# Kernel optimization log

Hardware: AMD Instinct MI355X
Metric: run time of the kernel (lower is better)

The kernel has to match this reference:

```python
import jax, jax.numpy as jnp
import numpy as np

B, H, T, TE = 48, 256, 512, 256  # batch*nodes, hidden=node_dim, timesteps, time_emb_dim


def timestep_embedding(ts, dim, max_positions=10000):
    half = dim // 2
    freqs = jnp.exp(jnp.arange(half, dtype=jnp.float32) * (-np.log(max_positions) / (half - 1)))
    e = ts.astype(jnp.float32)[:, None] * freqs[None, :]
    return jnp.concatenate([jnp.sin(e), jnp.cos(e)], axis=-1)  # [len, dim]


def mlp2(x, W1, b1, W2, b2):
    # 2-layer MLP: Linear -> SiLU -> Linear
    return jax.nn.silu(x @ W1 + b1) @ W2 + b2


def setup_inputs() -> dict:
    key = jax.random.key(0)
    ks = jax.random.split(key, 16)
    s = lambda k, shp, fan: (jax.random.normal(k, shp, dtype=jnp.float32) / np.sqrt(fan))
    return {
        "x": jax.random.normal(ks[0], (B, 3, T), dtype=jnp.float32),
        "h": jax.random.normal(ks[1], (B, H, T), dtype=jnp.float32),
        "qW1": s(ks[2], (H, H), H), "qb1": jnp.zeros((H,), jnp.float32),
        "qW2": s(ks[3], (H, H), H), "qb2": jnp.zeros((H,), jnp.float32),
        "kW1": s(ks[4], (H, H), H), "kb1": jnp.zeros((H,), jnp.float32),
        "kW2": s(ks[5], (H, H), H), "kb2": jnp.zeros((H,), jnp.float32),
        "vW1": s(ks[6], (H, H), H), "vb1": jnp.zeros((H,), jnp.float32),
        "vW2": s(ks[7], (H, H), H), "vb2": jnp.zeros((H,), jnp.float32),
        "xW1": s(ks[8], (H, H), H), "xb1": jnp.zeros((H,), jnp.float32),
        "xW2": s(ks[9], (H, 1), H), "xb2": jnp.zeros((1,), jnp.float32),
        "teW": s(ks[10], (TE, H), TE), "teb": jnp.zeros((H,), jnp.float32),
    }


def reference(x, h, qW1, qb1, qW2, qb2, kW1, kb1, kW2, kb2,
              vW1, vb1, vW2, vb2, xW1, xb1, xW2, xb2, teW, teb):
    Bb, _, Tt = x.shape
    rel_range = jnp.arange(-Tt + 1, Tt)
    emb_rel = timestep_embedding(rel_range, teW.shape[0]) @ teW + teb  # [2T-1, H]
    idx = jnp.arange(Tt)[:, None] - jnp.arange(Tt)[None, :] + (Tt - 1)  # [T, T]
    rel_pos = emb_rel[idx]  # [T, T, H]

    hm = h.transpose(0, 2, 1).reshape(Bb * Tt, -1)  # merge_time_dim: [BT, H]
    q = mlp2(hm, qW1, qb1, qW2, qb2)
    k = mlp2(hm, kW1, kb1, kW2, kb2)
    v = mlp2(hm, vW1, vb1, vW2, vb2)
    v_x = mlp2(v, xW1, xb1, xW2, xb2)  # [BT, 1]

    qt = q.reshape(Bb, Tt, -1)   # [B, T, H]
    kt = k.reshape(Bb, Tt, -1)
    vt = v.reshape(Bb, Tt, -1)

    base = jnp.einsum('bth,bsh->bts', qt, kt)  # [B, T, T]
    rel_logits = qt @ emb_rel.T  # [B, T, 2T-1]
    bias_logits = jnp.take_along_axis(
        rel_logits, jnp.broadcast_to(idx[None], (Bb, Tt, Tt)), axis=2)
    alpha = jax.nn.softmax(base + bias_logits, axis=-1)  # [B, T, T]

    std_vs = jnp.einsum('bts,bsh->bht', alpha, vt)       # [B, H, T]
    bias_h = jnp.einsum('bts,tsh->bht', alpha, rel_pos)  # [B, H, T]
    h_new = h + std_vs + bias_h

    # equivariant coord update: sum_s alpha[b,t,s]*(x[b,c,t]-x[b,c,s])*v_x[b,s]
    vx = v_x.reshape(Bb, Tt)               # [B, T]
    w = alpha * vx[:, None, :]             # [B, T, T]
    x_update = x * jnp.sum(w, axis=-1)[:, None, :] - jnp.einsum('bts,bcs->bct', w, x)
    x_new = x + x_update
    return (x_new, h_new)
```

## Files before the change

### kernel.cpp

```cpp
#include <hip/hip_runtime.h>
#include <math.h>

#define NB 48
#define HD 256
#define TS 512

typedef _Float16 f16x8 __attribute__((ext_vector_type(8)));
typedef float    f32x4 __attribute__((ext_vector_type(4)));

__device__ inline unsigned short f2h(float f) {
  union { _Float16 h; unsigned short u; } v; v.h = (_Float16)f; return v.u;
}
__device__ inline float h2f(unsigned short u) {
  union { unsigned short u; _Float16 h; } v; v.u = u; return (float)v.h;
}

#define ETS 1056

__device__ __forceinline__ void gll16(const void* g, void* l) {
  __builtin_amdgcn_global_load_lds(
      (const __attribute__((address_space(1))) unsigned int*)g,
      (__attribute__((address_space(3))) unsigned int*)l, 16, 0, 0);
}

__global__ __launch_bounds__(256) void k_embrel(
    const float* __restrict__ teW, const float* __restrict__ teb,
    unsigned short* __restrict__ embB, unsigned short* __restrict__ embT)
{
  __shared__ float e[256];
  const int r = blockIdx.x;
  const int tid = threadIdx.x;
  if (r == 1023) {
    embB[1023 * 256 + tid] = 0;
    for (int c = 1023; c < ETS; ++c) embT[(size_t)tid * ETS + c] = 0;
    return;
  }
  const float rel = (float)(r - (TS - 1));
  if (tid < 128) {
    float f = expf((float)tid * (-9.210340371976184f / 127.0f));
    float ang = rel * f;
    e[tid] = sinf(ang);
    e[tid + 128] = cosf(ang);
  }
  __syncthreads();
  float acc = teb[tid];
  for (int kk = 0; kk < 256; ++kk)
    acc = fmaf(e[kk], teW[kk * 256 + tid], acc);
  unsigned short hv = f2h(acc);
  embB[r * 256 + tid] = hv;
  embT[(size_t)tid * ETS + r] = hv;
}

__global__ __launch_bounds__(256) void k_prep_h(
    const float* __restrict__ h, unsigned short* __restrict__ hmH,
    float* __restrict__ vxZ)
{
  __shared__ float t[32 * 132];
  const int t0 = blockIdx.x * 128, c0 = blockIdx.y * 32, b = blockIdx.z;
  const int tid = threadIdx.x;
  if (blockIdx.y == 0 && blockIdx.z == 0) {
    float4* vz = (float4*)(vxZ + ((size_t)blockIdx.x * 256 + tid) * 24);
#pragma unroll
    for (int i = 0; i < 6; ++i) vz[i] = make_float4(0.f, 0.f, 0.f, 0.f);
  }
#pragma unroll
  for (int i = 0; i < 4; ++i) {
    int cl = i * 8 + (tid >> 5);
    int t4 = (tid & 31) * 4;
    float4 v = *(const float4*)&h[((size_t)b * 256 + c0 + cl) * 512 + t0 + t4];
    t[cl * 132 + t4 + 0] = v.x; t[cl * 132 + t4 + 1] = v.y;
    t[cl * 132 + t4 + 2] = v.z; t[cl * 132 + t4 + 3] = v.w;
  }
  __syncthreads();
#pragma unroll
  for (int i = 0; i < 16; ++i) {
    int tl = i * 8 + (tid >> 5);
    int cl = tid & 31;
    hmH[((size_t)b * 512 + t0 + tl) * 256 + c0 + cl] = f2h(t[cl * 132 + tl]);
  }
}

__global__ __launch_bounds__(256) void k_prep_w(
    const float* __restrict__ w0, const float* __restrict__ w1,
    const float* __restrict__ w2, const float* __restrict__ w3,
    const float* __restrict__ w4, const float* __restrict__ w5,
    const float* __restrict__ w6, unsigned short* __restrict__ WtH)
{
  __shared__ float t[64 * 68];
  const int mat = blockIdx.z;
  const float* W = (mat == 0) ? w0 : (mat == 1) ? w1 : (mat == 2) ? w2 :
                   (mat == 3) ? w3 : (mat == 4) ? w4 : (mat == 5) ? w5 : w6;
  unsigned short* dst = WtH + (size_t)mat * 65536;
  const int k0 = blockIdx.x * 64, n0 = blockIdx.y * 64;
  const int tid = threadIdx.x;
#pragma unroll
  for (int i = 0; i < 4; ++i) {
    int kr = i * 16 + (tid >> 4);
    int nc = (tid & 15) * 4;
    float4 v = *(const float4*)&W[(size_t)(k0 + kr) * 256 + n0 + nc];
    t[kr * 68 + nc + 0] = v.x; t[kr * 68 + nc + 1] = v.y;
    t[kr * 68 + nc + 2] = v.z; t[kr * 68 + nc + 3] = v.w;
  }
  __syncthreads();
#pragma unroll
  for (int i = 0; i < 4; ++i) {
    int nr = i * 16 + (tid >> 4);
    int kc = (tid & 15) * 4;
#pragma unroll
    for (int j = 0; j < 4; ++j)
      dst[(size_t)(n0 + nr) * 256 + k0 + kc + j] = f2h(t[(kc + j) * 68 + nr]);
  }
}

struct GJob {
  const unsigned short* A; const unsigned short* Wt; const float* bias;
  unsigned short* outB; unsigned short* outT;
  const float* vxW; float* vxOut;
};
struct GJobs { GJob j[3]; };

template<int ACT>
__global__ __launch_bounds__(512) void k_gemm(GJobs jobs)
{
  __shared__ __align__(16) char AsB[16384];
  __shared__ __align__(16) char WsB[32768];

  const GJob jb = jobs.j[blockIdx.z];

  const int tid  = threadIdx.x;
  const int lane = tid & 63;
  const int w    = tid >> 6;
  const int wr   = w >> 2, wc = w & 3;
  const int rq   = lane & 15;
  const int kq   = lane >> 4;

  const int m0 = blockIdx.x * 128;
  const char* Ag = (const char*)jb.A + (size_t)m0 * 512;
  const char* Wg = (const char*)jb.Wt;

  f32x4 acc[4][4];
#pragma unroll
  for (int mi = 0; mi < 4; ++mi)
#pragma unroll
    for (int ni = 0; ni < 4; ++ni)
      acc[mi][ni] = (f32x4){0.f, 0.f, 0.f, 0.f};

  for (int kt = 0; kt < 4; ++kt) {
    __syncthreads();
#pragma unroll
    for (int i = 0; i < 2; ++i) {
      int c = i * 512 + tid;
      int row = c >> 3, ch = c & 7;
      int colg = (ch * 16) ^ ((row & 7) << 4);
      gll16(Ag + (size_t)row * 512 + kt * 128 + colg, AsB + i * 8192 + w * 1024);
    }
#pragma unroll
    for (int i = 0; i < 4; ++i) {
      int c = i * 512 + tid;
      int row = c >> 3, ch = c & 7;
      int colg = (ch * 16) ^ ((row & 7) << 4);
      gll16(Wg + (size_t)row * 512 + kt * 128 + colg, WsB + i * 8192 + w * 1024);
    }
    __syncthreads();

#pragma unroll
    for (int ks = 0; ks < 2; ++ks) {
      const int kb = ks * 64 + kq * 16;
      f16x8 af[4], bfr[4];
#pragma unroll
      for (int mi = 0; mi < 4; ++mi) {
        int row = wr * 64 + mi * 16 + rq;
        af[mi] = *(const f16x8*)(AsB + row * 128 + (kb ^ ((row & 7) << 4)));
      }
#pragma unroll
      for (int ni = 0; ni < 4; ++ni) {
        int row = wc * 64 + ni * 16 + rq;
        bfr[ni] = *(const f16x8*)(WsB + row * 128 + (kb ^ ((row & 7) << 4)));
      }
#pragma unroll
      for (int mi = 0; mi < 4; ++mi)
#pragma unroll
        for (int ni = 0; ni < 4; ++ni)
          acc[mi][ni] = __builtin_amdgcn_mfma_f32_16x16x32_f16(
              af[mi], bfr[ni], acc[mi][ni], 0, 0, 0);
    }
  }

  float bv[4];
#pragma unroll
  for (int ni = 0; ni < 4; ++ni)
    bv[ni] = jb.bias[wc * 64 + ni * 16 + rq];

  float vxp_[4][4];
#pragma unroll
  for (int mi = 0; mi < 4; ++mi)
#pragma unroll
    for (int j = 0; j < 4; ++j) vxp_[mi][j] = 0.f;

  const int bb = m0 >> 9;
  const int tbase = (m0 & 511) + wr * 64;

#pragma unroll
  for (int mi = 0; mi < 4; ++mi) {
#pragma unroll
    for (int ni = 0; ni < 4; ++ni) {
      const int n = wc * 64 + ni * 16 + rq;
      float vl4[4];
#pragma unroll
      for (int j = 0; j < 4; ++j) {
        float vl = acc[mi][ni][j] + bv[ni];
        if (ACT) vl = vl / (1.0f + __expf(-vl));
        vl4[j] = vl;
      }
      if (jb.outB) {
        const int m = m0 + wr * 64 + mi * 16 + kq * 4;
#pragma unroll
        for (int j = 0; j < 4; ++j)
          jb.outB[(size_t)(m + j) * 256 + n] = f2h(vl4[j]);
      }
      if (jb.outT) {
        ushort4 o;
        o.x = f2h(vl4[0]); o.y = f2h(vl4[1]);
        o.z = f2h(vl4[2]); o.w = f2h(vl4[3]);
        *(ushort4*)&jb.outT[((size_t)(bb * 256 + n) << 9) +
                            tbase + mi * 16 + kq * 4] = o;
      }
      if (jb.vxOut) {
        float wq = jb.vxW[n];
#pragma unroll
        for (int j = 0; j < 4; ++j) vxp_[mi][j] = fmaf(vl4[j], wq, vxp_[mi][j]);
      }
    }
  }

  if (jb.vxOut) {
#pragma unroll
    for (int mi = 0; mi < 4; ++mi)
#pragma unroll
      for (int j = 0; j < 4; ++j) {
        float s = vxp_[mi][j];
        s += __shfl_xor(s, 1); s += __shfl_xor(s, 2);
        s += __shfl_xor(s, 4); s += __shfl_xor(s, 8);
        if (rq == 0)
          atomicAdd(&jb.vxOut[m0 + wr * 64 + mi * 16 + kq * 4 + j], s);
      }
  }
}

__global__ __launch_bounds__(256, 2) void k_attn6(
    const float* __restrict__ xin, const float* __restrict__ hin,
    const unsigned short* __restrict__ qH, const unsigned short* __restrict__ kH,
    const unsigned short* __restrict__ vtH, const float* __restrict__ vxm,
    const float* __restrict__ xb2p,
    const unsigned short* __restrict__ embB, const unsigned short* __restrict__ embT,
    float* __restrict__ xout, float* __restrict__ hout)
{
  __shared__ __align__(16) char smem[70656];
  float* S  = (float*)smem;
  unsigned short* Pb = (unsigned short*)smem;
  unsigned short* Pe = (unsigned short*)(smem + 33280);

  const int tid  = threadIdx.x;
  const int lane = tid & 63;
  const int w    = tid >> 6;
  const int rq   = lane & 15;
  const int kq   = lane >> 4;
  const int id = blockIdx.x;
  const int t0 = ((id >> 3) & 15) * 32;
  const int b  = (id & 7) + 8 * (id >> 7);
  const int sw = w * 128;

  f16x8 q0[8], q1[8];
  {
    const size_t qo = ((size_t)(b * TS + t0 + rq) << 8) + kq * 8;
#pragma unroll
    for (int ks = 0; ks < 8; ++ks) {
      q0[ks] = *(const f16x8*)(qH + qo + ks * 32);
      q1[ks] = *(const f16x8*)(qH + qo + 4096 + ks * 32);
    }
  }

  f32x4 a0[8], a1[8];
#pragma unroll
  for (int ni = 0; ni < 8; ++ni) {
    a0[ni] = (f32x4){0.f, 0.f, 0.f, 0.f};
    a1[ni] = (f32x4){0.f, 0.f, 0.f, 0.f};
  }
  {
    const unsigned short* kp = kH + ((size_t)(b * TS + sw + rq) << 8) + kq * 8;
    f16x8 kA[8], kB[8];
#pragma unroll
    for (int ni = 0; ni < 8; ++ni) kA[ni] = *(const f16x8*)(kp + ni * 4096);
#pragma unroll
    for (int ni = 0; ni < 8; ++ni) kB[ni] = *(const f16x8*)(kp + ni * 4096 + 32);
#pragma unroll
    for (int ks = 0; ks < 8; ks += 2) {
#pragma unroll
      for (int ni = 0; ni < 8; ++ni) {
        a0[ni] = __builtin_amdgcn_mfma_f32_16x16x32_f16(q0[ks], kA[ni], a0[ni], 0, 0, 0);
        a1[ni] = __builtin_amdgcn_mfma_f32_16x16x32_f16(q1[ks], kA[ni], a1[ni], 0, 0, 0);
        if (ks + 2 < 8) kA[ni] = *(const f16x8*)(kp + ni * 4096 + (ks + 2) * 32);
      }
#pragma unroll
      for (int ni = 0; ni < 8; ++ni) {
        a0[ni] = __builtin_amdgcn_mfma_f32_16x16x32_f16(q0[ks + 1], kB[ni], a0[ni], 0, 0, 0);
        a1[ni] = __builtin_amdgcn_mfma_f32_16x16x32_f16(q1[ks + 1], kB[ni], a1[ni], 0, 0, 0);
        if (ks + 3 < 8) kB[ni] = *(const f16x8*)(kp + ni * 4096 + (ks + 3) * 32);
      }
    }
  }

  const int rbR = t0 - sw + 384;
  const unsigned short* ep = embB + ((size_t)(rbR + rq) << 8) + kq * 8;
  f16x8 eA[10], eB[10];
#pragma unroll
  for (int f = 0; f < 10; ++f) eA[f] = *(const f16x8*)(ep + f * 4096);
#pragma unroll
  for (int ni = 0; ni < 8; ++ni)
#pragma unroll
    for (int j = 0; j < 4; ++j) {
      S[(kq * 4 + j) * 524 + sw + ni * 16 + rq]        = a0[ni][j];
      S[(16 + kq * 4 + j) * 524 + sw + ni * 16 + rq]   = a1[ni][j];
    }
#pragma unroll
  for (int f = 0; f < 10; ++f) eB[f] = *(const f16x8*)(ep + f * 4096 + 32);

  f32x4 r0[9], r1[9];
#pragma unroll
  for (int ni = 0; ni < 9; ++ni) {
    r0[ni] = (f32x4){0.f, 0.f, 0.f, 0.f};
    r1[ni] = (f32x4){0.f, 0.f, 0.f, 0.f};
  }
#pragma unroll
  for (int ks = 0; ks < 8; ks += 2) {
#pragma unroll
    for (int f = 0; f < 10; ++f) {
      if (f < 9) r0[f] = __builtin_amdgcn_mfma_f32_16x16x32_f16(q0[ks], eA[f], r0[f], 0, 0, 0);
      if (f > 0) r1[f - 1] = __builtin_amdgcn_mfma_f32_16x16x32_f16(q1[ks], eA[f], r1[f - 1], 0, 0, 0);
      if (ks + 2 < 8) eA[f] = *(const f16x8*)(ep + f * 4096 + (ks + 2) * 32);
    }
#pragma unroll
    for (int f = 0; f < 10; ++f) {
      if (f < 9) r0[f] = __builtin_amdgcn_mfma_f32_16x16x32_f16(q0[ks + 1], eB[f], r0[f], 0, 0, 0);
      if (f > 0) r1[f - 1] = __builtin_amdgcn_mfma_f32_16x16x32_f16(q1[ks + 1], eB[f], r1[f - 1], 0, 0, 0);
      if (ks + 3 < 8) eB[f] = *(const f16x8*)(ep + f * 4096 + (ks + 3) * 32);
    }
  }

  asm volatile("s_waitcnt lgkmcnt(0)" ::: "memory");
  __builtin_amdgcn_sched_barrier(0);
#pragma unroll
  for (int ni = 0; ni < 9; ++ni)
#pragma unroll
    for (int j = 0; j < 4; ++j) {
      int tp  = kq * 4 + j;
      int slw = tp + 127 - (ni * 16 + rq);
      if (slw >= 0 && slw < 128) {
        S[tp * 524 + sw + slw]        += r0[ni][j];
        S[(16 + tp) * 524 + sw + slw] += r1[ni][j];
      }
    }
  __syncthreads();

  const int row16 = tid >> 4, tx = tid & 15;
  float p0[32], p1[32];
  float invl0, invl1;
#pragma unroll
  for (int pass = 0; pass < 2; ++pass) {
    float* pp = pass ? p1 : p0;
    const float* Srow = S + (pass * 16 + row16) * 524 + tx * 4;
    float mx = -3.0e38f, l = 0.f;
#pragma unroll
    for (int i = 0; i < 8; ++i) {
      float4 v = *(const float4*)(Srow + i * 64);
      pp[4*i+0] = v.x; pp[4*i+1] = v.y; pp[4*i+2] = v.z; pp[4*i+3] = v.w;
    }
#pragma unroll
    for (int i = 0; i < 32; ++i) mx = fmaxf(mx, pp[i]);
    mx = fmaxf(mx, __shfl_xor(mx, 1)); mx = fmaxf(mx, __shfl_xor(mx, 2));
    mx = fmaxf(mx, __shfl_xor(mx, 4)); mx = fmaxf(mx, __shfl_xor(mx, 8));
#pragma unroll
    for (int i = 0; i < 32; ++i) { pp[i] = __expf(pp[i] - mx); l += pp[i]; }
    l += __shfl_xor(l, 1); l += __shfl_xor(l, 2);
    l += __shfl_xor(l, 4); l += __shfl_xor(l, 8);
    if (pass) invl1 = 1.0f / l; else invl0 = 1.0f / l;
  }

  {
    const float xb2c = xb2p[0];
    const float* vxp = vxm + b * TS;
    const float* xp  = xin + (size_t)b * 3 * TS;
    float w0s = 0.f, xa00 = 0.f, xa01 = 0.f, xa02 = 0.f;
    float w1s = 0.f, xa10 = 0.f, xa11 = 0.f, xa12 = 0.f;
#pragma unroll
    for (int i = 0; i < 8; ++i) {
      int s = i * 64 + tx * 4;
      float4 vv = *(const float4*)(vxp + s);
      float4 x0 = *(const float4*)(xp + s);
      float4 x1 = *(const float4*)(xp + TS + s);
      float4 x2 = *(const float4*)(xp + 2 * TS + s);
      float vb0 = vv.x + xb2c, vb1 = vv.y + xb2c, vb2 = vv.z + xb2c, vb3 = vv.w + xb2c;
      float wv;
      wv = p0[4*i+0] * vb0; w0s += wv; xa00 = fmaf(wv, x0.x, xa00); xa01 = fmaf(wv, x1.x, xa01); xa02 = fmaf(wv, x2.x, xa02);
      wv = p0[4*i+1] * vb1; w0s += wv; xa00 = fmaf(wv, x0.y, xa00); xa01 = fmaf(wv, x1.y, xa01); xa02 = fmaf(wv, x2.y, xa02);
      wv = p0[4*i+2] * vb2; w0s += wv; xa00 = fmaf(wv, x0.z, xa00); xa01 = fmaf(wv, x1.z, xa01); xa02 = fmaf(wv, x2.z, xa02);
      wv = p0[4*i+3] * vb3; w0s += wv; xa00 = fmaf(wv, x0.w, xa00); xa01 = fmaf(wv, x1.w, xa01); xa02 = fmaf(wv, x2.w, xa02);
      wv = p1[4*i+0] * vb0; w1s += wv; xa10 = fmaf(wv, x0.x, xa10); xa11 = fmaf(wv, x1.x, xa11); xa12 = fmaf(wv, x2.x, xa12);
      wv = p1[4*i+1] * vb1; w1s += wv; xa10 = fmaf(wv, x0.y, xa10); xa11 = fmaf(wv, x1.y, xa11); xa12 = fmaf(wv, x2.y, xa12);
      wv = p1[4*i+2] * vb2; w1s += wv; xa10 = fmaf(wv, x0.z, xa10); xa11 = fmaf(wv, x1.z, xa11); xa12 = fmaf(wv, x2.z, xa12);
      wv = p1[4*i+3] * vb3; w1s += wv; xa10 = fmaf(wv, x0.w, xa10); xa11 = fmaf(wv, x1.w, xa11); xa12 = fmaf(wv, x2.w, xa12);
    }
#pragma unroll
    for (int m = 1; m < 16; m <<= 1) {
      w0s += __shfl_xor(w0s, m); xa00 += __shfl_xor(xa00, m);
      xa01 += __shfl_xor(xa01, m); xa02 += __shfl_xor(xa02, m);
      w1s += __shfl_xor(w1s, m); xa10 += __shfl_xor(xa10, m);
      xa11 += __shfl_xor(xa11, m); xa12 += __shfl_xor(xa12, m);
    }
    if (tx == 0) {
      int ta = t0 + row16, tb2 = t0 + 16 + row16;
      float wsa = w0s * invl0, wsb = w1s * invl1;
      xout[(b * 3 + 0) * TS + ta] = xp[ta]          * (1.0f + wsa) - xa00 * invl0;
      xout[(b * 3 + 1) * TS + ta] = xp[TS + ta]     * (1.0f + wsa) - xa01 * invl0;
      xout[(b * 3 + 2) * TS + ta] = xp[2 * TS + ta] * (1.0f + wsa) - xa02 * invl0;
      xout[(b * 3 + 0) * TS + tb2] = xp[tb2]          * (1.0f + wsb) - xa10 * invl1;
      xout[(b * 3 + 1) * TS + tb2] = xp[TS + tb2]     * (1.0f + wsb) - xa11 * invl1;
      xout[(b * 3 + 2) * TS + tb2] = xp[2 * TS + tb2] * (1.0f + wsb) - xa12 * invl1;
    }
  }
  __syncthreads();

  {
    unsigned int* pz = (unsigned int*)Pe;
    for (int i = tid; i < 9344; i += 256) pz[i] = 0u;
  }
  __syncthreads();

#pragma unroll
  for (int pass = 0; pass < 2; ++pass) {
    const float* pp = pass ? p1 : p0;
    const float il = pass ? invl1 : invl0;
    const int row = pass * 16 + row16;
    unsigned short* pbrow = Pb + row * 520 + tx * 4;
    unsigned short* perow = Pe + row * 584 + row + 511;
#pragma unroll
    for (int i = 0; i < 8; ++i) {
      int s = i * 64 + tx * 4;
      ushort4 pu;
      pu.x = f2h(pp[4*i+0] * il); pu.y = f2h(pp[4*i+1] * il);
      pu.z = f2h(pp[4*i+2] * il); pu.w = f2h(pp[4*i+3] * il);
      *(ushort4*)(pbrow + i * 64) = pu;
      perow[-(s + 0)] = pu.x; perow[-(s + 1)] = pu.y;
      perow[-(s + 2)] = pu.z; perow[-(s + 3)] = pu.w;
    }
  }
  __syncthreads();

  const int n0 = w * 64;
  f32x4 o0[4], o1[4];
#pragma unroll
  for (int ni = 0; ni < 4; ++ni) {
    o0[ni] = (f32x4){0.f, 0.f, 0.f, 0.f};
    o1[ni] = (f32x4){0.f, 0.f, 0.f, 0.f};
  }
  {
    const unsigned short* pb0 = Pb + rq * 520 + kq * 8;
    const unsigned short* pb1 = Pb + (16 + rq) * 520 + kq * 8;
    const unsigned short* pe0 = Pe + rq * 584 + kq * 8;
    const unsigned short* pe1 = Pe + (16 + rq) * 584 + kq * 8;
    const unsigned short* vtp = vtH + ((size_t)(b * 256 + n0 + rq) << 9) + kq * 8;
    const unsigned short* etp = embT + (size_t)(n0 + rq) * ETS + t0 + kq * 8;
    f16x8 vA[4], vB[4], gA[4], gB[4];
#pragma unroll
    for (int ni = 0; ni < 4; ++ni) {
      vA[ni] = *(const f16x8*)(vtp + ni * 8192);
      gA[ni] = *(const f16x8*)(etp + ni * 16 * ETS);
      vB[ni] = *(const f16x8*)(vtp + ni * 8192 + 32);
      gB[ni] = *(const f16x8*)(etp + ni * 16 * ETS + 32);
    }
#pragma unroll
    for (int kk = 0; kk < 16; kk += 2) {
      f16x8 pa0 = *(const f16x8*)(pb0 + kk * 32);
      f16x8 pa1 = *(const f16x8*)(pb1 + kk * 32);
#pragma unroll
      for (int ni = 0; ni < 4; ++ni) {
        o0[ni] = __builtin_amdgcn_mfma_f32_16x16x32_f16(pa0, vA[ni], o0[ni], 0, 0, 0);
        o1[ni] = __builtin_amdgcn_mfma_f32_16x16x32_f16(pa1, vA[ni], o1[ni], 0, 0, 0);
        if (kk + 2 < 16) vA[ni] = *(const f16x8*)(vtp + ni * 8192 + (kk + 2) * 32);
      }
      f16x8 pe0f = *(const f16x8*)(pe0 + kk * 32);
      f16x8 pe1f = *(const f16x8*)(pe1 + kk * 32);
#pragma unroll
      for (int ni = 0; ni < 4; ++ni) {
        o0[ni] = __builtin_amdgcn_mfma_f32_16x16x32_f16(pe0f, gA[ni], o0[ni], 0, 0, 0);
        o1[ni] = __builtin_amdgcn_mfma_f32_16x16x32_f16(pe1f, gA[ni], o1[ni], 0, 0, 0);
        if (kk + 2 < 17) gA[ni] = *(const f16x8*)(etp + ni * 16 * ETS + (kk + 2) * 32);
      }
      f16x8 pc0 = *(const f16x8*)(pb0 + (kk + 1) * 32);
      f16x8 pc1 = *(const f16x8*)(pb1 + (kk + 1) * 32);
#pragma unroll
      for (int ni = 0; ni < 4; ++ni) {
        o0[ni] = __builtin_amdgcn_mfma_f32_16x16x32_f16(pc0, vB[ni], o0[ni], 0, 0, 0);
        o1[ni] = __builtin_amdgcn_mfma_f32_16x16x32_f16(pc1, vB[ni], o1[ni], 0, 0, 0);
        if (kk + 3 < 16) vB[ni] = *(const f16x8*)(vtp + ni * 8192 + (kk + 3) * 32);
      }
      f16x8 pd0 = *(const f16x8*)(pe0 + (kk + 1) * 32);
      f16x8 pd1 = *(const f16x8*)(pe1 + (kk + 1) * 32);
#pragma unroll
      for (int ni = 0; ni < 4; ++ni) {
        o0[ni] = __builtin_amdgcn_mfma_f32_16x16x32_f16(pd0, gB[ni], o0[ni], 0, 0, 0);
        o1[ni] = __builtin_amdgcn_mfma_f32_16x16x32_f16(pd1, gB[ni], o1[ni], 0, 0, 0);
        if (kk + 3 < 17) gB[ni] = *(const f16x8*)(etp + ni * 16 * ETS + (kk + 3) * 32);
      }
    }
    f16x8 pt0 = *(const f16x8*)(pe0 + 16 * 32);
    f16x8 pt1 = *(const f16x8*)(pe1 + 16 * 32);
#pragma unroll
    for (int ni = 0; ni < 4; ++ni) {
      o0[ni] = __builtin_amdgcn_mfma_f32_16x16x32_f16(pt0, gA[ni], o0[ni], 0, 0, 0);
      o1[ni] = __builtin_amdgcn_mfma_f32_16x16x32_f16(pt1, gA[ni], o1[ni], 0, 0, 0);
    }
  }

  {
#pragma unroll
    for (int ni = 0; ni < 4; ++ni) {
      int hh = n0 + ni * 16 + rq;
      size_t base = (((size_t)(b * 256 + hh)) << 9) + t0 + kq * 4;
      float4 hv0 = *(const float4*)(hin + base);
      float4 ov0;
      ov0.x = hv0.x + o0[ni][0];
      ov0.y = hv0.y + o0[ni][1];
      ov0.z = hv0.z + o0[ni][2];
      ov0.w = hv0.w + o0[ni][3];
      *(float4*)(hout + base) = ov0;
      float4 hv1 = *(const float4*)(hin + base + 16);
      float4 ov1;
      ov1.x = hv1.x + o1[ni][0];
      ov1.y = hv1.y + o1[ni][1];
      ov1.z = hv1.z + o1[ni][2];
      ov1.w = hv1.w + o1[ni][3];
      *(float4*)(hout + base + 16) = ov1;
    }
  }
}

extern "C" void kernel_launch(void* const* d_in, const int* in_sizes, int n_in,
                              void* d_out, int out_size, void* d_ws, size_t ws_size,
                              hipStream_t stream)
{
  const float* x   = (const float*)d_in[0];
  const float* h   = (const float*)d_in[1];
  const float* qW1 = (const float*)d_in[2];
  const float* qb1 = (const float*)d_in[3];
  const float* qW2 = (const float*)d_in[4];
  const float* qb2 = (const float*)d_in[5];
  const float* kW1 = (const float*)d_in[6];
  const float* kb1 = (const float*)d_in[7];
  const float* kW2 = (const float*)d_in[8];
  const float* kb2 = (const float*)d_in[9];
  const float* vW1 = (const float*)d_in[10];
  const float* vb1 = (const float*)d_in[11];
  const float* vW2 = (const float*)d_in[12];
  const float* vb2 = (const float*)d_in[13];
  const float* xW1 = (const float*)d_in[14];
  const float* xb1 = (const float*)d_in[15];
  const float* xW2 = (const float*)d_in[16];
  const float* xb2 = (const float*)d_in[17];
  const float* teW = (const float*)d_in[18];
  const float* teb = (const float*)d_in[19];

  unsigned short* cur = (unsigned short*)d_ws;
  unsigned short* embB = cur; cur += 1024 * 256;
  unsigned short* embT = cur; cur += 256 * ETS;
  unsigned short* hmH  = cur; cur += (size_t)24576 * 256;
  unsigned short* WtH  = cur; cur += 7 * 65536;
  unsigned short* hidQ = cur; cur += (size_t)24576 * 256;
  unsigned short* hidK = cur; cur += (size_t)24576 * 256;
  unsigned short* hidV = cur; cur += (size_t)24576 * 256;
  unsigned short* qHp  = cur; cur += (size_t)24576 * 256;
  unsigned short* kHp  = cur; cur += (size_t)24576 * 256;
  unsigned short* vHp  = cur; cur += (size_t)24576 * 256;
  unsigned short* vtH  = cur; cur += (size_t)24576 * 256;
  float* vx = (float*)cur;

  float* xout = (float*)d_out;
  float* hout = xout + NB * 3 * TS;

  k_embrel<<<1024, 256, 0, stream>>>(teW, teb, embB, embT);
  k_prep_h<<<dim3(4, 8, 48), 256, 0, stream>>>(h, hmH, vx);
  k_prep_w<<<dim3(4, 4, 7), 256, 0, stream>>>(qW1, qW2, kW1, kW2, vW1, vW2, xW1, WtH);

  {
    GJobs j1{{{hmH, WtH + 0 * 65536, qb1, hidQ, nullptr, nullptr, nullptr},
              {hmH, WtH + 2 * 65536, kb1, hidK, nullptr, nullptr, nullptr},
              {hmH, WtH + 4 * 65536, vb1, hidV, nullptr, nullptr, nullptr}}};
    k_gemm<1><<<dim3(192, 1, 3), 512, 0, stream>>>(j1);
    GJobs j2{{{hidQ, WtH + 1 * 65536, qb2, qHp, nullptr, nullptr, nullptr},
              {hidK, WtH + 3 * 65536, kb2, kHp, nullptr, nullptr, nullptr},
              {hidV, WtH + 5 * 65536, vb2, vHp, vtH, nullptr, nullptr}}};
    k_gemm<0><<<dim3(192, 1, 3), 512, 0, stream>>>(j2);
  }
  {
    GJobs j3{{{vHp, WtH + 6 * 65536, xb1, nullptr, nullptr, xW2, vx},
              {}, {}}};
    k_gemm<1><<<dim3(192, 1, 1), 512, 0, stream>>>(j3);
  }

  k_attn6<<<768, 256, 0, stream>>>(x, h, qHp, kHp, vtH, vx, xb2,
                                   embB, embT, xout, hout);
}
```

Before: 217.3 us.

## Fuse two-layer MLPs in LDS, merge prep kernels, compute rel embedding with MFMA

```diff
diff --git a/kernel.cpp b/kernel.cpp
--- a/kernel.cpp
+++ b/kernel.cpp
@@ -23,109 +23,252 @@
       (__attribute__((address_space(3))) unsigned int*)l, 16, 0, 0);
 }
 
-__global__ __launch_bounds__(256) void k_embrel(
-    const float* __restrict__ teW, const float* __restrict__ teb,
-    unsigned short* __restrict__ embB, unsigned short* __restrict__ embT)
-{
-  __shared__ float e[256];
-  const int r = blockIdx.x;
-  const int tid = threadIdx.x;
-  if (r == 1023) {
-    embB[1023 * 256 + tid] = 0;
-    for (int c = 1023; c < ETS; ++c) embT[(size_t)tid * ETS + c] = 0;
-    return;
-  }
-  const float rel = (float)(r - (TS - 1));
-  if (tid < 128) {
-    float f = expf((float)tid * (-9.210340371976184f / 127.0f));
-    float ang = rel * f;
-    e[tid] = sinf(ang);
-    e[tid + 128] = cosf(ang);
-  }
-  __syncthreads();
-  float acc = teb[tid];
-  for (int kk = 0; kk < 256; ++kk)
-    acc = fmaf(e[kk], teW[kk * 256 + tid], acc);
-  unsigned short hv = f2h(acc);
-  embB[r * 256 + tid] = hv;
-  embT[(size_t)tid * ETS + r] = hv;
-}
-
-__global__ __launch_bounds__(256) void k_prep_h(
+__global__ __launch_bounds__(256) void k_prep(
     const float* __restrict__ h, unsigned short* __restrict__ hmH,
-    float* __restrict__ vxZ)
-{
-  __shared__ float t[32 * 132];
-  const int t0 = blockIdx.x * 128, c0 = blockIdx.y * 32, b = blockIdx.z;
-  const int tid = threadIdx.x;
-  if (blockIdx.y == 0 && blockIdx.z == 0) {
-    float4* vz = (float4*)(vxZ + ((size_t)blockIdx.x * 256 + tid) * 24);
-#pragma unroll
-    for (int i = 0; i < 6; ++i) vz[i] = make_float4(0.f, 0.f, 0.f, 0.f);
-  }
-#pragma unroll
-  for (int i = 0; i < 4; ++i) {
-    int cl = i * 8 + (tid >> 5);
-    int t4 = (tid & 31) * 4;
-    float4 v = *(const float4*)&h[((size_t)b * 256 + c0 + cl) * 512 + t0 + t4];
-    t[cl * 132 + t4 + 0] = v.x; t[cl * 132 + t4 + 1] = v.y;
-    t[cl * 132 + t4 + 2] = v.z; t[cl * 132 + t4 + 3] = v.w;
-  }
-  __syncthreads();
-#pragma unroll
-  for (int i = 0; i < 16; ++i) {
-    int tl = i * 8 + (tid >> 5);
-    int cl = tid & 31;
-    hmH[((size_t)b * 512 + t0 + tl) * 256 + c0 + cl] = f2h(t[cl * 132 + tl]);
-  }
-}
-
-__global__ __launch_bounds__(256) void k_prep_w(
+    float* __restrict__ vxZ,
     const float* __restrict__ w0, const float* __restrict__ w1,
     const float* __restrict__ w2, const float* __restrict__ w3,
     const float* __restrict__ w4, const float* __restrict__ w5,
-    const float* __restrict__ w6, unsigned short* __restrict__ WtH)
+    const float* __restrict__ w6, const float* __restrict__ w7,
+    unsigned short* __restrict__ WtH, unsigned short* __restrict__ SC)
 {
-  __shared__ float t[64 * 68];
-  const int mat = blockIdx.z;
-  const float* W = (mat == 0) ? w0 : (mat == 1) ? w1 : (mat == 2) ? w2 :
-                   (mat == 3) ? w3 : (mat == 4) ? w4 : (mat == 5) ? w5 : w6;
-  unsigned short* dst = WtH + (size_t)mat * 65536;
-  const int k0 = blockIdx.x * 64, n0 = blockIdx.y * 64;
+  const int gid = blockIdx.x;
   const int tid = threadIdx.x;
-#pragma unroll
-  for (int i = 0; i < 4; ++i) {
-    int kr = i * 16 + (tid >> 4);
-    int nc = (tid & 15) * 4;
-    float4 v = *(const float4*)&W[(size_t)(k0 + kr) * 256 + n0 + nc];
-    t[kr * 68 + nc + 0] = v.x; t[kr * 68 + nc + 1] = v.y;
-    t[kr * 68 + nc + 2] = v.z; t[kr * 68 + nc + 3] = v.w;
-  }
-  __syncthreads();
-#pragma unroll
-  for (int i = 0; i < 4; ++i) {
-    int nr = i * 16 + (tid >> 4);
-    int kc = (tid & 15) * 4;
-#pragma unroll
-    for (int j = 0; j < 4; ++j)
-      dst[(size_t)(n0 + nr) * 256 + k0 + kc + j] = f2h(t[(kc + j) * 68 + nr]);
+
+  if (gid < 128) {
+    const int cf = tid & 127, half = tid >> 7;
+    const float f = expf((float)cf * (-9.210340371976184f / 127.0f));
+#pragma unroll
+    for (int rr = 0; rr < 8; ++rr) {
+      int r = gid * 8 + rr;
+      float ang = (float)(r - (TS - 1)) * f;
+      float val = (r == 1023) ? 0.0f : (half ? cosf(ang) : sinf(ang));
+      SC[r * 256 + tid] = f2h(val);
+    }
+    return;
+  }
+  if (gid < 1664) {
+    const int idx = gid - 128;
+    const int bx = idx & 3, by = (idx >> 2) & 7, bz = idx >> 5;
+    __shared__ float t[32 * 132];
+    const int t0 = bx * 128, c0 = by * 32, b = bz;
+    if (by == 0 && bz == 0) {
+      float4* vz = (float4*)(vxZ + ((size_t)bx * 256 + tid) * 24);
+#pragma unroll
+      for (int i = 0; i < 6; ++i) vz[i] = make_float4(0.f, 0.f, 0.f, 0.f);
+    }
+#pragma unroll
+    for (int i = 0; i < 4; ++i) {
+      int cl = i * 8 + (tid >> 5);
+      int t4 = (tid & 31) * 4;
+      float4 v = *(const float4*)&h[((size_t)b * 256 + c0 + cl) * 512 + t0 + t4];
+      t[cl * 132 + t4 + 0] = v.x; t[cl * 132 + t4 + 1] = v.y;
+      t[cl * 132 + t4 + 2] = v.z; t[cl * 132 + t4 + 3] = v.w;
+    }
+    __syncthreads();
+#pragma unroll
+    for (int i = 0; i < 16; ++i) {
+      int tl = i * 8 + (tid >> 5);
+      int cl = tid & 31;
+      hmH[((size_t)b * 512 + t0 + tl) * 256 + c0 + cl] = f2h(t[cl * 132 + tl]);
+    }
+    return;
+  }
+  {
+    const int idx = gid - 1664;
+    const int kx = idx & 3, ny = (idx >> 2) & 3, mat = idx >> 4;
+    const float* W = (mat == 0) ? w0 : (mat == 1) ? w1 : (mat == 2) ? w2 :
+                     (mat == 3) ? w3 : (mat == 4) ? w4 : (mat == 5) ? w5 :
+                     (mat == 6) ? w6 : w7;
+    unsigned short* dst = WtH + (size_t)mat * 65536;
+    __shared__ float t[64 * 68];
+    const int k0 = kx * 64, n0 = ny * 64;
+#pragma unroll
+    for (int i = 0; i < 4; ++i) {
+      int kr = i * 16 + (tid >> 4);
+      int nc = (tid & 15) * 4;
+      float4 v = *(const float4*)&W[(size_t)(k0 + kr) * 256 + n0 + nc];
+      t[kr * 68 + nc + 0] = v.x; t[kr * 68 + nc + 1] = v.y;
+      t[kr * 68 + nc + 2] = v.z; t[kr * 68 + nc + 3] = v.w;
+    }
+    __syncthreads();
+#pragma unroll
+    for (int i = 0; i < 4; ++i) {
+      int nr = i * 16 + (tid >> 4);
+      int kc = (tid & 15) * 4;
+#pragma unroll
+      for (int j = 0; j < 4; ++j)
+        dst[(size_t)(n0 + nr) * 256 + k0 + kc + j] = f2h(t[(kc + j) * 68 + nr]);
+    }
+  }
+}
+
+struct MJob {
+  const unsigned short* A; const unsigned short* W1; const float* b1;
+  const unsigned short* W2; const float* b2;
+  unsigned short* outB; unsigned short* outT;
+};
+struct MJobs { MJob j[3]; };
+
+__global__ __launch_bounds__(256) void k_mlp2(MJobs jobs)
+{
+  __shared__ __align__(16) char Wst[32768];
+  __shared__ __align__(16) char Ast[8192];
+  __shared__ __align__(16) char Hst[64 * 528];
+
+  const MJob jb = jobs.j[blockIdx.y];
+  const int tid  = threadIdx.x;
+  const int lane = tid & 63;
+  const int w    = tid >> 6;
+  const int rq   = lane & 15;
+  const int kq   = lane >> 4;
+  const int m0   = blockIdx.x * 64;
+  const char* Ag  = (const char*)jb.A  + (size_t)m0 * 512;
+  const char* W1g = (const char*)jb.W1;
+  const char* W2g = (const char*)jb.W2;
+
+  f32x4 acc[4][4];
+#pragma unroll
+  for (int mi = 0; mi < 4; ++mi)
+#pragma unroll
+    for (int ni = 0; ni < 4; ++ni) acc[mi][ni] = (f32x4){0.f, 0.f, 0.f, 0.f};
+
+  for (int kt = 0; kt < 4; ++kt) {
+    __syncthreads();
+#pragma unroll
+    for (int i = 0; i < 2; ++i) {
+      int c = i * 256 + tid;
+      int row = c >> 3, ch = c & 7;
+      int colg = (ch * 16) ^ ((row & 7) << 4);
+      gll16(Ag + (size_t)row * 512 + kt * 128 + colg, Ast + i * 4096 + w * 1024);
+    }
+#pragma unroll
+    for (int i = 0; i < 8; ++i) {
+      int c = i * 256 + tid;
+      int row = c >> 3, ch = c & 7;
+      int colg = (ch * 16) ^ ((row & 7) << 4);
+      gll16(W1g + (size_t)row * 512 + kt * 128 + colg, Wst + i * 4096 + w * 1024);
+    }
+    __syncthreads();
+#pragma unroll
+    for (int ks = 0; ks < 2; ++ks) {
+      const int kb = ks * 64 + kq * 16;
+      f16x8 af[4], bfr[4];
+#pragma unroll
+      for (int mi = 0; mi < 4; ++mi) {
+        int row = mi * 16 + rq;
+        af[mi] = *(const f16x8*)(Ast + row * 128 + (kb ^ ((row & 7) << 4)));
+      }
+#pragma unroll
+      for (int ni = 0; ni < 4; ++ni) {
+        int row = w * 64 + ni * 16 + rq;
+        bfr[ni] = *(const f16x8*)(Wst + row * 128 + (kb ^ ((row & 7) << 4)));
+      }
+#pragma unroll
+      for (int mi = 0; mi < 4; ++mi)
+#pragma unroll
+        for (int ni = 0; ni < 4; ++ni)
+          acc[mi][ni] = __builtin_amdgcn_mfma_f32_16x16x32_f16(
+              af[mi], bfr[ni], acc[mi][ni], 0, 0, 0);
+    }
+  }
+  {
+#pragma unroll
+    for (int ni = 0; ni < 4; ++ni) {
+      const int n = w * 64 + ni * 16 + rq;
+      const float bv = jb.b1[n];
+#pragma unroll
+      for (int mi = 0; mi < 4; ++mi)
+#pragma unroll
+        for (int j = 0; j < 4; ++j) {
+          float vl = acc[mi][ni][j] + bv;
+          vl = vl / (1.0f + __expf(-vl));
+          int m = mi * 16 + kq * 4 + j;
+          *(unsigned short*)(Hst + m * 528 + n * 2) = f2h(vl);
+        }
+    }
+  }
+#pragma unroll
+  for (int mi = 0; mi < 4; ++mi)
+#pragma unroll
+    for (int ni = 0; ni < 4; ++ni) acc[mi][ni] = (f32x4){0.f, 0.f, 0.f, 0.f};
+
+  for (int kt = 0; kt < 4; ++kt) {
+    __syncthreads();
+#pragma unroll
+    for (int i = 0; i < 8; ++i) {
+      int c = i * 256 + tid;
+      int row = c >> 3, ch = c & 7;
+      int colg = (ch * 16) ^ ((row & 7) << 4);
+      gll16(W2g + (size_t)row * 512 + kt * 128 + colg, Wst + i * 4096 + w * 1024);
+    }
+    __syncthreads();
+#pragma unroll
+    for (int ks = 0; ks < 2; ++ks) {
+      const int kb = ks * 64 + kq * 16;
+      f16x8 af[4], bfr[4];
+#pragma unroll
+      for (int mi = 0; mi < 4; ++mi) {
+        int row = mi * 16 + rq;
+        af[mi] = *(const f16x8*)(Hst + row * 528 + kt * 128 + kb);
+      }
+#pragma unroll
+      for (int ni = 0; ni < 4; ++ni) {
+        int row = w * 64 + ni * 16 + rq;
+        bfr[ni] = *(const f16x8*)(Wst + row * 128 + (kb ^ ((row & 7) << 4)));
+      }
+#pragma unroll
+      for (int mi = 0; mi < 4; ++mi)
+#pragma unroll
+        for (int ni = 0; ni < 4; ++ni)
+          acc[mi][ni] = __builtin_amdgcn_mfma_f32_16x16x32_f16(
+              af[mi], bfr[ni], acc[mi][ni], 0, 0, 0);
+    }
+  }
+
+  const int bb = m0 >> 9;
+  const int tbase = m0 & 511;
+#pragma unroll
+  for (int ni = 0; ni < 4; ++ni) {
+    const int n = w * 64 + ni * 16 + rq;
+    const float bv = jb.b2[n];
+#pragma unroll
+    for (int mi = 0; mi < 4; ++mi) {
+      float vl4[4];
+#pragma unroll
+      for (int j = 0; j < 4; ++j) vl4[j] = acc[mi][ni][j] + bv;
+#pragma unroll
+      for (int j = 0; j < 4; ++j) {
+        int m = m0 + mi * 16 + kq * 4 + j;
+        jb.outB[(size_t)m * 256 + n] = f2h(vl4[j]);
+      }
+      if (jb.outT) {
+        ushort4 o;
+        o.x = f2h(vl4[0]); o.y = f2h(vl4[1]);
+        o.z = f2h(vl4[2]); o.w = f2h(vl4[3]);
+        *(ushort4*)&jb.outT[((size_t)(bb * 256 + n) << 9) +
+                            tbase + mi * 16 + kq * 4] = o;
+      }
+    }
   }
 }
 
 struct GJob {
   const unsigned short* A; const unsigned short* Wt; const float* bias;
-  unsigned short* outB; unsigned short* outT;
+  unsigned short* outB; unsigned short* outE;
   const float* vxW; float* vxOut;
+  int act; int mMax;
 };
-struct GJobs { GJob j[3]; };
-
-template<int ACT>
+struct GJobs { GJob j[2]; };
+
 __global__ __launch_bounds__(512) void k_gemm(GJobs jobs)
 {
   __shared__ __align__(16) char AsB[16384];
   __shared__ __align__(16) char WsB[32768];
 
   const GJob jb = jobs.j[blockIdx.z];
+  const int m0 = blockIdx.x * 128;
+  if (m0 >= jb.mMax) return;
 
   const int tid  = threadIdx.x;
   const int lane = tid & 63;
@@ -134,7 +277,6 @@
   const int rq   = lane & 15;
   const int kq   = lane >> 4;
 
-  const int m0 = blockIdx.x * 128;
   const char* Ag = (const char*)jb.A + (size_t)m0 * 512;
   const char* Wg = (const char*)jb.Wt;
 
@@ -142,8 +284,7 @@
 #pragma unroll
   for (int mi = 0; mi < 4; ++mi)
 #pragma unroll
-    for (int ni = 0; ni < 4; ++ni)
-      acc[mi][ni] = (f32x4){0.f, 0.f, 0.f, 0.f};
+    for (int ni = 0; ni < 4; ++ni) acc[mi][ni] = (f32x4){0.f, 0.f, 0.f, 0.f};
 
   for (int kt = 0; kt < 4; ++kt) {
     __syncthreads();
@@ -162,7 +303,6 @@
       gll16(Wg + (size_t)row * 512 + kt * 128 + colg, WsB + i * 8192 + w * 1024);
     }
     __syncthreads();
-
 #pragma unroll
     for (int ks = 0; ks < 2; ++ks) {
       const int kb = ks * 64 + kq * 16;
@@ -197,9 +337,6 @@
 #pragma unroll
     for (int j = 0; j < 4; ++j) vxp_[mi][j] = 0.f;
 
-  const int bb = m0 >> 9;
-  const int tbase = (m0 & 511) + wr * 64;
-
 #pragma unroll
   for (int mi = 0; mi < 4; ++mi) {
 #pragma unroll
@@ -209,21 +346,19 @@
 #pragma unroll
       for (int j = 0; j < 4; ++j) {
         float vl = acc[mi][ni][j] + bv[ni];
-        if (ACT) vl = vl / (1.0f + __expf(-vl));
+        if (jb.act) vl = vl / (1.0f + __expf(-vl));
         vl4[j] = vl;
       }
+      const int mb = m0 + wr * 64 + mi * 16 + kq * 4;
       if (jb.outB) {
-        const int m = m0 + wr * 64 + mi * 16 + kq * 4;
 #pragma unroll
         for (int j = 0; j < 4; ++j)
-          jb.outB[(size_t)(m + j) * 256 + n] = f2h(vl4[j]);
-      }
-      if (jb.outT) {
-        ushort4 o;
-        o.x = f2h(vl4[0]); o.y = f2h(vl4[1]);
-        o.z = f2h(vl4[2]); o.w = f2h(vl4[3]);
-        *(ushort4*)&jb.outT[((size_t)(bb * 256 + n) << 9) +
-                            tbase + mi * 16 + kq * 4] = o;
+          jb.outB[(size_t)(mb + j) * 256 + n] = f2h(vl4[j]);
+      }
+      if (jb.outE) {
+#pragma unroll
+        for (int j = 0; j < 4; ++j)
+          jb.outE[(size_t)n * ETS + mb + j] = f2h(vl4[j]);
       }
       if (jb.vxOut) {
         float wq = jb.vxW[n];
@@ -573,11 +708,9 @@
   unsigned short* cur = (unsigned short*)d_ws;
   unsigned short* embB = cur; cur += 1024 * 256;
   unsigned short* embT = cur; cur += 256 * ETS;
+  unsigned short* SC   = cur; cur += 1024 * 256;
   unsigned short* hmH  = cur; cur += (size_t)24576 * 256;
-  unsigned short* WtH  = cur; cur += 7 * 65536;
-  unsigned short* hidQ = cur; cur += (size_t)24576 * 256;
-  unsigned short* hidK = cur; cur += (size_t)24576 * 256;
-  unsigned short* hidV = cur; cur += (size_t)24576 * 256;
+  unsigned short* WtH  = cur; cur += 8 * 65536;
   unsigned short* qHp  = cur; cur += (size_t)24576 * 256;
   unsigned short* kHp  = cur; cur += (size_t)24576 * 256;
   unsigned short* vHp  = cur; cur += (size_t)24576 * 256;
@@ -587,24 +720,21 @@
   float* xout = (float*)d_out;
   float* hout = xout + NB * 3 * TS;
 
-  k_embrel<<<1024, 256, 0, stream>>>(teW, teb, embB, embT);
-  k_prep_h<<<dim3(4, 8, 48), 256, 0, stream>>>(h, hmH, vx);
-  k_prep_w<<<dim3(4, 4, 7), 256, 0, stream>>>(qW1, qW2, kW1, kW2, vW1, vW2, xW1, WtH);
-
-  {
-    GJobs j1{{{hmH, WtH + 0 * 65536, qb1, hidQ, nullptr, nullptr, nullptr},
-              {hmH, WtH + 2 * 65536, kb1, hidK, nullptr, nullptr, nullptr},
-              {hmH, WtH + 4 * 65536, vb1, hidV, nullptr, nullptr, nullptr}}};
-    k_gemm<1><<<dim3(192, 1, 3), 512, 0, stream>>>(j1);
-    GJobs j2{{{hidQ, WtH + 1 * 65536, qb2, qHp, nullptr, nullptr, nullptr},
-              {hidK, WtH + 3 * 65536, kb2, kHp, nullptr, nullptr, nullptr},
-              {hidV, WtH + 5 * 65536, vb2, vHp, vtH, nullptr, nullptr}}};
-    k_gemm<0><<<dim3(192, 1, 3), 512, 0, stream>>>(j2);
-  }
-  {
-    GJobs j3{{{vHp, WtH + 6 * 65536, xb1, nullptr, nullptr, xW2, vx},
-              {}, {}}};
-    k_gemm<1><<<dim3(192, 1, 1), 512, 0, stream>>>(j3);
+  k_prep<<<1792, 256, 0, stream>>>(h, hmH, vx,
+                                   qW1, qW2, kW1, kW2, vW1, vW2, xW1, teW,
+                                   WtH, SC);
+
+  {
+    MJobs jm{{{hmH, WtH + 0 * 65536, qb1, WtH + 1 * 65536, qb2, qHp, nullptr},
+              {hmH, WtH + 2 * 65536, kb1, WtH + 3 * 65536, kb2, kHp, nullptr},
+              {hmH, WtH + 4 * 65536, vb1, WtH + 5 * 65536, vb2, vHp, vtH}}};
+    k_mlp2<<<dim3(384, 3), 256, 0, stream>>>(jm);
+  }
+
+  {
+    GJobs jg{{{SC,  WtH + 7 * 65536, teb, embB, embT, nullptr, nullptr, 0, 1024},
+              {vHp, WtH + 6 * 65536, xb1, nullptr, nullptr, xW2, vx, 1, 24576}}};
+    k_gemm<<<dim3(192, 1, 2), 512, 0, stream>>>(jg);
   }
 
   k_attn6<<<768, 256, 0, stream>>>(x, h, qHp, kHp, vtH, vx, xb2,
```

Measured after the change: 190.2 us (median of 2 runs). 1.14x faster.
